# Kernel tuning notes

Measured on AMD Instinct MI355X. Metric: run time of the kernel, lower is better.

## Reference

```python
import jax, jax.numpy as jnp
import numpy as np

D_MODEL = 1024
N_HEADS = 16
D_K = D_MODEL // N_HEADS
LN_EPS = 1e-5


def setup_inputs() -> dict:
    key = jax.random.key(0)
    ks = jax.random.split(key, 11)
    s = 1.0 / np.sqrt(D_MODEL)
    x = jax.random.normal(ks[0], (4, 2048, D_MODEL), dtype=jnp.float32)
    W_q = jax.random.uniform(ks[1], (D_MODEL, D_MODEL), jnp.float32, -s, s)
    b_q = jax.random.uniform(ks[2], (D_MODEL,), jnp.float32, -s, s)
    W_k = jax.random.uniform(ks[3], (D_MODEL, D_MODEL), jnp.float32, -s, s)
    b_k = jax.random.uniform(ks[4], (D_MODEL,), jnp.float32, -s, s)
    W_v = jax.random.uniform(ks[5], (D_MODEL, D_MODEL), jnp.float32, -s, s)
    b_v = jax.random.uniform(ks[6], (D_MODEL,), jnp.float32, -s, s)
    W_o = jax.random.uniform(ks[7], (D_MODEL, D_MODEL), jnp.float32, -s, s)
    b_o = jax.random.uniform(ks[8], (D_MODEL,), jnp.float32, -s, s)
    ln_gamma = jnp.ones((D_MODEL,), jnp.float32)
    ln_beta = jnp.zeros((D_MODEL,), jnp.float32)
    return {"x": x, "W_q": W_q, "b_q": b_q, "W_k": W_k, "b_k": b_k,
            "W_v": W_v, "b_v": b_v, "W_o": W_o, "b_o": b_o,
            "ln_gamma": ln_gamma, "ln_beta": ln_beta}


def reference(x, W_q, b_q, W_k, b_k, W_v, b_v, W_o, b_o, ln_gamma, ln_beta):
    B, S, D = x.shape
    # Linear projections (torch Linear: x @ W.T + b); split into heads.
    def proj(W, b):
        y = jnp.einsum('bsd,ed->bse', x, W) + b
        return y.reshape(B, S, N_HEADS, D_K).transpose(0, 2, 1, 3)  # [B,H,S,dk]
    Q = proj(W_q, b_q)
    K = proj(W_k, b_k)
    V = proj(W_v, b_v)
    scores = jnp.einsum('bhqd,bhkd->bhqk', Q, K) / np.sqrt(D_K)
    attn = jax.nn.softmax(scores, axis=-1)  # dropout is identity in eval
    context = jnp.einsum('bhqk,bhkd->bhqd', attn, V)
    context = context.transpose(0, 2, 1, 3).reshape(B, S, D)
    out = jnp.einsum('bsd,ed->bse', context, W_o) + b_o
    h = x + out  # residual
    mu = jnp.mean(h, axis=-1, keepdims=True)
    var = jnp.mean(jnp.square(h - mu), axis=-1, keepdims=True)
    return (h - mu) / jnp.sqrt(var + LN_EPS) * ln_gamma + ln_beta
```

## Files before the change

### kernel.cpp

```cpp
#include <hip/hip_runtime.h>
#include <hip/hip_bf16.h>
#include <stdint.h>

typedef __attribute__((ext_vector_type(4))) float f32x4;
typedef __attribute__((ext_vector_type(8))) short bf16x8;
typedef __attribute__((ext_vector_type(4))) short bf16x4;
typedef __attribute__((ext_vector_type(4))) short s16x4;

__device__ __forceinline__ float b2f(short s) {
    union { uint32_t u; float f; } v; v.u = ((uint32_t)(uint16_t)s) << 16; return v.f;
}
__device__ __forceinline__ short f2b(float f) {
    union { float f; uint32_t u; } v; v.f = f;
    uint32_t r = v.u + 0x7FFF + ((v.u >> 16) & 1);
    return (short)(r >> 16);
}
__device__ __forceinline__ f32x4 zero4() { f32x4 z = {0.f, 0.f, 0.f, 0.f}; return z; }

__device__ __forceinline__ void async16(const void* g, void* l) {
    __builtin_amdgcn_global_load_lds(
        (const __attribute__((address_space(1))) void*)g,
        (__attribute__((address_space(3))) void*)l, 16, 0, 0);
}
__device__ __forceinline__ uint32_t lds_addr(const void* p) {
    return (uint32_t)(uintptr_t)(const __attribute__((address_space(3))) void*)p;
}
__device__ __forceinline__ float exp2fast(float x) {
    float r; asm("v_exp_f32 %0, %1" : "=v"(r) : "v"(x)); return r;
}
__device__ __forceinline__ uint32_t cvtpk(float lo, float hi) {
    uint32_t r; asm("v_cvt_pk_bf16_f32 %0, %1, %2" : "=v"(r) : "v"(lo), "v"(hi)); return r;
}

__global__ __launch_bounds__(256)
void cvt5(const float* __restrict__ x,
          const float* __restrict__ wq, const float* __restrict__ wk,
          const float* __restrict__ wv, const float* __restrict__ wo,
          short* __restrict__ xb, short* __restrict__ wqb, short* __restrict__ wkb,
          short* __restrict__ wvb, short* __restrict__ wob)
{
    const int b = blockIdx.x;
    const float* src; short* dst; size_t off;
    if (b < 8192) { src = x; dst = xb; off = (size_t)b * 1024; }
    else {
        const int wsel = (b - 8192) >> 10;
        off = (size_t)((b - 8192) & 1023) * 1024;
        switch (wsel) {
            case 0: src = wq; dst = wqb; break;
            case 1: src = wk; dst = wkb; break;
            case 2: src = wv; dst = wvb; break;
            default: src = wo; dst = wob; break;
        }
    }
    const int t = threadIdx.x;
    const float4 v = *(const float4*)(src + off + t * 4);
    s16x4 o;
    o[0] = f2b(v.x); o[1] = f2b(v.y); o[2] = f2b(v.z); o[3] = f2b(v.w);
    *(s16x4*)(dst + off + t * 4) = o;
}

template <bool OUTF32, bool RESID>
__device__ __forceinline__
void gemm_core(const short* __restrict__ Ab, const short* __restrict__ Bb,
               const float* __restrict__ bias, const float* __restrict__ resid,
               void* __restrict__ Cv, int m0, int n0col, int K, int N,
               short* lsA, short* lsB)
{
    const int t = threadIdx.x;
    const int wave = t >> 6, lane = t & 63;
    const int wr = wave >> 1, wc = wave & 1;
    const int lr = lane & 15, kg = lane >> 4;

    f32x4 acc[4][4];
#pragma unroll
    for (int m = 0; m < 4; ++m)
#pragma unroll
        for (int n = 0; n < 4; ++n) acc[m][n] = zero4();

    const int rG = t >> 3;
    const int cG = (((t & 7) ^ (rG & 7))) * 8;

    for (int k0 = 0; k0 < K; k0 += 64) {
        __syncthreads();
#pragma unroll
        for (int i = 0; i < 4; ++i) {
            async16(Ab + (size_t)(rG + 32 * i) * K + k0 + cG, &lsA[t * 8 + 2048 * i]);
            async16(Bb + (size_t)(rG + 32 * i) * K + k0 + cG, &lsB[t * 8 + 2048 * i]);
        }
        __syncthreads();

#pragma unroll
        for (int ks = 0; ks < 2; ++ks) {
            const int xc = ((ks * 4 + kg) ^ (lr & 7)) * 8;
            bf16x8 aF[4], bF[4];
#pragma unroll
            for (int m = 0; m < 4; ++m)
                aF[m] = *(const bf16x8*)&lsA[(wr * 64 + m * 16 + lr) * 64 + xc];
#pragma unroll
            for (int n = 0; n < 4; ++n)
                bF[n] = *(const bf16x8*)&lsB[(wc * 64 + n * 16 + lr) * 64 + xc];
#pragma unroll
            for (int m = 0; m < 4; ++m)
#pragma unroll
                for (int n = 0; n < 4; ++n)
                    acc[m][n] = __builtin_amdgcn_mfma_f32_16x16x32_bf16(aF[m], bF[n], acc[m][n], 0, 0, 0);
        }
    }

#pragma unroll
    for (int n = 0; n < 4; ++n) {
        const int col = n0col + wc * 64 + n * 16 + lr;
        const float bvv = bias[col];
#pragma unroll
        for (int m = 0; m < 4; ++m) {
            const int rowb = m0 + wr * 64 + m * 16 + kg * 4;
#pragma unroll
            for (int r = 0; r < 4; ++r) {
                const size_t idx = (size_t)(rowb + r) * N + col;
                float v = acc[m][n][r] + bvv;
                if (RESID) v += resid[idx];
                if (OUTF32) ((float*)Cv)[idx] = v;
                else        ((short*)Cv)[idx] = f2b(v);
            }
        }
    }
}

__global__ __launch_bounds__(256)
void gemm_qkv(const short* __restrict__ A, const short* __restrict__ Wcat,
              const float* __restrict__ bq, const float* __restrict__ bk,
              const float* __restrict__ bv,
              short* __restrict__ Qw, short* __restrict__ Kw, short* __restrict__ Vw)
{
    __shared__ short lsA[128 * 64];
    __shared__ short lsB[128 * 64];
    const int nb = blockIdx.x;
    const int tb = nb >> 3;
    const float* bias = (tb == 0) ? bq : (tb == 1) ? bk : bv;
    short* dst = (tb == 0) ? Qw : (tb == 1) ? Kw : Vw;
    gemm_core<false, false>(A + (size_t)blockIdx.y * 128 * 1024,
                            Wcat + (size_t)nb * 128 * 1024,
                            bias - (nb & 7) * 128,
                            nullptr, dst, blockIdx.y * 128, (nb & 7) * 128, 1024, 1024,
                            lsA, lsB);
}

__global__ __launch_bounds__(256)
void gemm_out(const short* __restrict__ A, const short* __restrict__ Bw,
              const float* __restrict__ bias, const float* __restrict__ resid,
              float* __restrict__ C)
{
    __shared__ short lsA[128 * 64];
    __shared__ short lsB[128 * 64];
    gemm_core<true, true>(A + (size_t)blockIdx.y * 128 * 1024,
                          Bw + (size_t)blockIdx.x * 128 * 1024,
                          bias, resid, C, blockIdx.y * 128, blockIdx.x * 128, 1024, 1024,
                          lsA, lsB);
}

__global__ __launch_bounds__(512)
void attn_fwd(const short* __restrict__ Q, const short* __restrict__ K,
              const short* __restrict__ V, short* __restrict__ ctx)
{
    __shared__ short lsK[2][64 * 64];
    __shared__ short lsV[2][64 * 64];
    __shared__ short lsP[8][16 * 64];

    const float C1 = 0.18033688011112042f;

    const int t = threadIdx.x, w = t >> 6, lane = t & 63;
    const int lr = lane & 15, kg = lane >> 4;
    const int bh = blockIdx.x;
    const size_t base = (size_t)(bh >> 4) * 2048 * 1024 + (size_t)(bh & 15) * 64;
    const short* Qg = Q + base;
    short* Og = ctx + base;
    const int q0 = blockIdx.y * 256 + w * 32;

    bf16x8 qB[2][2];
#pragma unroll
    for (int m = 0; m < 2; ++m)
#pragma unroll
        for (int ks = 0; ks < 2; ++ks)
            qB[m][ks] = *(const bf16x8*)(Qg + (size_t)(q0 + m * 16 + lr) * 1024 + ks * 32 + kg * 8);

    const int rK  = t >> 3;
    const int cK  = (((t & 7) ^ (rK & 7))) * 8;
    const int kvV = (t & 127) >> 1;
    const int dV  = ((t >> 7) << 4) + (t & 1) * 8;
    const short* pK = K + base + (size_t)rK * 1024 + cK;
    const short* pV = V + base + (size_t)kvV * 1024 + dV;

    f32x4 o[2][4];
#pragma unroll
    for (int m = 0; m < 2; ++m)
#pragma unroll
        for (int n = 0; n < 4; ++n) o[m][n] = zero4();
    float mx[2] = {-1e30f, -1e30f};
    float lsum[2] = {0.f, 0.f};

    const int pmask = (lr & 7) << 3;
    short* lsPw = lsP[w];

    async16(pK, &lsK[0][t * 8]);
    async16(pV, &lsV[0][t * 8]);

    int buf = 0;
    for (int it = 0; it < 32; ++it) {
        __syncthreads();
        if (it + 1 < 32) {
            pK += 65536; pV += 65536;
            async16(pK, &lsK[buf ^ 1][t * 8]);
            async16(pV, &lsV[buf ^ 1][t * 8]);
        }
        const short* cbK = lsK[buf];
        const short* cbV = lsV[buf];

        f32x4 s[2][4];
        const int x0 = ((kg)     ^ (lr & 7)) * 8;
        const int x1 = ((4 + kg) ^ (lr & 7)) * 8;
        __builtin_amdgcn_s_setprio(1);
#pragma unroll
        for (int cb = 0; cb < 4; ++cb) {
            const bf16x8 kA0 = *(const bf16x8*)&cbK[(cb * 16 + lr) * 64 + x0];
            const bf16x8 kA1 = *(const bf16x8*)&cbK[(cb * 16 + lr) * 64 + x1];
#pragma unroll
            for (int m = 0; m < 2; ++m) {
                f32x4 a = __builtin_amdgcn_mfma_f32_16x16x32_bf16(kA0, qB[m][0], zero4(), 0, 0, 0);
                s[m][cb] = __builtin_amdgcn_mfma_f32_16x16x32_bf16(kA1, qB[m][1], a, 0, 0, 0);
            }
        }
        __builtin_amdgcn_s_setprio(0);

        float smax[2];
#pragma unroll
        for (int m = 0; m < 2; ++m) {
            float a = fmaxf(fmaxf(s[m][0][0], s[m][0][1]), fmaxf(s[m][0][2], s[m][0][3]));
            float b = fmaxf(fmaxf(s[m][1][0], s[m][1][1]), fmaxf(s[m][1][2], s[m][1][3]));
            float c = fmaxf(fmaxf(s[m][2][0], s[m][2][1]), fmaxf(s[m][2][2], s[m][2][3]));
            float d = fmaxf(fmaxf(s[m][3][0], s[m][3][1]), fmaxf(s[m][3][2], s[m][3][3]));
            float e = fmaxf(fmaxf(a, b), fmaxf(c, d));
            e = fmaxf(e, __shfl_xor(e, 16));
            e = fmaxf(e, __shfl_xor(e, 32));
            smax[m] = e;
        }

        if (!__all((smax[0] <= mx[0] + 64.f) && (smax[1] <= mx[1] + 64.f))) {
            float corrS[2];
#pragma unroll
            for (int m = 0; m < 2; ++m) {
                const float mnew = fmaxf(mx[m], smax[m]);
                corrS[m] = exp2fast((mx[m] - mnew) * C1);
                mx[m] = mnew;
                lsum[m] *= corrS[m];
            }
#pragma unroll
            for (int m = 0; m < 2; ++m) {
                f32x4 c;
#pragma unroll
                for (int r = 0; r < 4; ++r) c[r] = __shfl(corrS[m], kg * 4 + r);
#pragma unroll
                for (int n = 0; n < 4; ++n) {
                    o[m][n][0] *= c[0]; o[m][n][1] *= c[1];
                    o[m][n][2] *= c[2]; o[m][n][3] *= c[3];
                }
            }
        }

        bf16x4 tv[4][4];
#pragma unroll
        for (int n = 0; n < 4; ++n) {
            const uint32_t a = lds_addr(&cbV[n * 1024 + kg * 128 + lr]);
            asm volatile(
                "ds_read_b64_tr_b16 %0, %4\n\t"
                "ds_read_b64_tr_b16 %1, %4 offset:128\n\t"
                "ds_read_b64_tr_b16 %2, %4 offset:1024\n\t"
                "ds_read_b64_tr_b16 %3, %4 offset:1152"
                : "=&v"(tv[n][0]), "=&v"(tv[n][1]), "=&v"(tv[n][2]), "=&v"(tv[n][3])
                : "v"(a));
        }
        asm volatile("s_waitcnt lgkmcnt(0)" ::: "memory");
        __builtin_amdgcn_sched_barrier(0);

#pragma unroll
        for (int m = 0; m < 2; ++m) {
            const float nm2 = mx[m] * C1;
            float tsum = 0.f;
#pragma unroll
            for (int cb = 0; cb < 4; ++cb) {
                const float p0 = exp2fast(fmaf(s[m][cb][0], C1, -nm2));
                const float p1 = exp2fast(fmaf(s[m][cb][1], C1, -nm2));
                const float p2 = exp2fast(fmaf(s[m][cb][2], C1, -nm2));
                const float p3 = exp2fast(fmaf(s[m][cb][3], C1, -nm2));
                tsum += (p0 + p1) + (p2 + p3);
                const int c0i = (cb * 16 + kg * 4) ^ pmask;
                *(uint32_t*)&lsPw[lr * 64 + c0i]     = cvtpk(p0, p1);
                *(uint32_t*)&lsPw[lr * 64 + c0i + 2] = cvtpk(p2, p3);
            }
            lsum[m] += tsum;

            bf16x8 pA[2];
#pragma unroll
            for (int kh = 0; kh < 2; ++kh)
                pA[kh] = *(const bf16x8*)&lsPw[lr * 64 + ((kh * 32 + kg * 8) ^ pmask)];

            __builtin_amdgcn_s_setprio(1);
#pragma unroll
            for (int n = 0; n < 4; ++n) {
#pragma unroll
                for (int kh = 0; kh < 2; ++kh) {
                    const bf16x8 vB = __builtin_shufflevector(tv[n][kh * 2], tv[n][kh * 2 + 1],
                                                              0, 1, 2, 3, 4, 5, 6, 7);
                    o[m][n] = __builtin_amdgcn_mfma_f32_16x16x32_bf16(pA[kh], vB, o[m][n], 0, 0, 0);
                }
            }
            __builtin_amdgcn_s_setprio(0);
        }
        buf ^= 1;
    }

#pragma unroll
    for (int m = 0; m < 2; ++m) {
        float lp = lsum[m];
        lp += __shfl_xor(lp, 16);
        lp += __shfl_xor(lp, 32);
        f32x4 inv;
#pragma unroll
        for (int r = 0; r < 4; ++r) inv[r] = 1.0f / __shfl(lp, kg * 4 + r);
#pragma unroll
        for (int n = 0; n < 4; ++n)
#pragma unroll
            for (int r = 0; r < 4; ++r) {
                const int row = q0 + m * 16 + kg * 4 + r;
                Og[(size_t)row * 1024 + n * 16 + lr] = f2b(o[m][n][r] * inv[r]);
            }
    }
}

__global__ __launch_bounds__(256)
void ln_inplace(float* __restrict__ io, const float* __restrict__ gamma,
                const float* __restrict__ beta)
{
    __shared__ float redS[4];
    __shared__ float redQ[4];
    const int t = threadIdx.x, wave = t >> 6, lane = t & 63;
    const size_t rb = (size_t)blockIdx.x * 1024;

    float4 v4 = *(const float4*)&io[rb + t * 4];
    float v[4] = {v4.x, v4.y, v4.z, v4.w};

    float s = 0.f, sq = 0.f;
#pragma unroll
    for (int j = 0; j < 4; ++j) { s += v[j]; sq += v[j] * v[j]; }
#pragma unroll
    for (int off = 32; off; off >>= 1) {
        s  += __shfl_xor(s, off);
        sq += __shfl_xor(sq, off);
    }
    if (lane == 0) { redS[wave] = s; redQ[wave] = sq; }
    __syncthreads();
    const float mean = (redS[0] + redS[1] + redS[2] + redS[3]) * (1.0f / 1024.0f);
    const float ex2  = (redQ[0] + redQ[1] + redQ[2] + redQ[3]) * (1.0f / 1024.0f);
    const float var  = fmaxf(ex2 - mean * mean, 0.f);
    const float inv  = rsqrtf(var + 1e-5f);

    float4 o4;
    o4.x = (v[0] - mean) * inv * gamma[t * 4 + 0] + beta[t * 4 + 0];
    o4.y = (v[1] - mean) * inv * gamma[t * 4 + 1] + beta[t * 4 + 1];
    o4.z = (v[2] - mean) * inv * gamma[t * 4 + 2] + beta[t * 4 + 2];
    o4.w = (v[3] - mean) * inv * gamma[t * 4 + 3] + beta[t * 4 + 3];
    *(float4*)&io[rb + t * 4] = o4;
}

extern "C" void kernel_launch(void* const* d_in, const int* in_sizes, int n_in,
                              void* d_out, int out_size, void* d_ws, size_t ws_size,
                              hipStream_t stream)
{
    const float* x  = (const float*)d_in[0];
    const float* Wq = (const float*)d_in[1];
    const float* bq = (const float*)d_in[2];
    const float* Wk = (const float*)d_in[3];
    const float* bk = (const float*)d_in[4];
    const float* Wv = (const float*)d_in[5];
    const float* bv = (const float*)d_in[6];
    const float* Wo = (const float*)d_in[7];
    const float* bo = (const float*)d_in[8];
    const float* gamma = (const float*)d_in[9];
    const float* beta  = (const float*)d_in[10];

    const size_t NX = (size_t)8192 * 1024;
    const size_t NW = (size_t)1024 * 1024;

    short* xb  = (short*)d_ws;
    short* Wqb = xb + NX;
    short* Wkb = Wqb + NW;
    short* Wvb = Wkb + NW;
    short* Wob = Wvb + NW;
    short* Qw  = Wob + NW;
    short* Kw  = Qw + NX;
    short* Vw  = Kw + NX;
    short* Cw  = Vw + NX;
    float* out = (float*)d_out;

    cvt5<<<dim3(12288), dim3(256), 0, stream>>>(x, Wq, Wk, Wv, Wo, xb, Wqb, Wkb, Wvb, Wob);
    gemm_qkv<<<dim3(24, 64), dim3(256), 0, stream>>>(xb, Wqb, bq, bk, bv, Qw, Kw, Vw);
    attn_fwd<<<dim3(64, 8), dim3(512), 0, stream>>>(Qw, Kw, Vw, Cw);
    gemm_out<<<dim3(8, 64), dim3(256), 0, stream>>>(Cw, Wob, bo, x, out);
    ln_inplace<<<dim3(8192), dim3(256), 0, stream>>>(out, gamma, beta);
}
```

Measured before the change: 243.5 us.

## Remap GEMM workgroups per XCD and compute softmax row sums via MFMA

Both GEMM kernels now launch a 1D grid and remap each block index so that consecutive tiles go to the same XCD (blocks are assigned round-robin over 8 XCDs). The aim is better L2 reuse of the A and B tiles. The attention kernel drops the scalar row-sum accumulation and its cross-lane shuffles. It instead multiplies the bf16 P tile by a ones vector with two extra MFMAs per row block, which moves the reduction onto the matrix units. The row sums now come from bf16-rounded probabilities, so they match what multiplies V, at the cost of extra MFMA work.

```diff
diff --git a/kernel.cpp b/kernel.cpp
--- a/kernel.cpp
+++ b/kernel.cpp
@@ -134,14 +134,17 @@
 {
     __shared__ short lsA[128 * 64];
     __shared__ short lsB[128 * 64];
-    const int nb = blockIdx.x;
+    const int L = blockIdx.x;
+    const int wgid = (L & 7) * 192 + (L >> 3);
+    const int nb = wgid % 24;
+    const int my = wgid / 24;
     const int tb = nb >> 3;
     const float* bias = (tb == 0) ? bq : (tb == 1) ? bk : bv;
     short* dst = (tb == 0) ? Qw : (tb == 1) ? Kw : Vw;
-    gemm_core<false, false>(A + (size_t)blockIdx.y * 128 * 1024,
+    gemm_core<false, false>(A + (size_t)my * 128 * 1024,
                             Wcat + (size_t)nb * 128 * 1024,
                             bias - (nb & 7) * 128,
-                            nullptr, dst, blockIdx.y * 128, (nb & 7) * 128, 1024, 1024,
+                            nullptr, dst, my * 128, (nb & 7) * 128, 1024, 1024,
                             lsA, lsB);
 }
 
@@ -152,9 +155,12 @@
 {
     __shared__ short lsA[128 * 64];
     __shared__ short lsB[128 * 64];
-    gemm_core<true, true>(A + (size_t)blockIdx.y * 128 * 1024,
-                          Bw + (size_t)blockIdx.x * 128 * 1024,
-                          bias, resid, C, blockIdx.y * 128, blockIdx.x * 128, 1024, 1024,
+    const int L = blockIdx.x;
+    const int wgid = (L & 7) * 64 + (L >> 3);
+    const int nb = wgid & 7, my = wgid >> 3;
+    gemm_core<true, true>(A + (size_t)my * 128 * 1024,
+                          Bw + (size_t)nb * 128 * 1024,
+                          bias, resid, C, my * 128, nb * 128, 1024, 1024,
                           lsA, lsB);
 }
 
@@ -183,6 +189,10 @@
         for (int ks = 0; ks < 2; ++ks)
             qB[m][ks] = *(const bf16x8*)(Qg + (size_t)(q0 + m * 16 + lr) * 1024 + ks * 32 + kg * 8);
 
+    bf16x8 onesB;
+#pragma unroll
+    for (int j = 0; j < 8; ++j) onesB[j] = (short)0x3F80;
+
     const int rK  = t >> 3;
     const int cK  = (((t & 7) ^ (rK & 7))) * 8;
     const int kvV = (t & 127) >> 1;
@@ -191,12 +201,14 @@
     const short* pV = V + base + (size_t)kvV * 1024 + dV;
 
     f32x4 o[2][4];
-#pragma unroll
-    for (int m = 0; m < 2; ++m)
+    f32x4 osum[2];
+#pragma unroll
+    for (int m = 0; m < 2; ++m) {
 #pragma unroll
         for (int n = 0; n < 4; ++n) o[m][n] = zero4();
+        osum[m] = zero4();
+    }
     float mx[2] = {-1e30f, -1e30f};
-    float lsum[2] = {0.f, 0.f};
 
     const int pmask = (lr & 7) << 3;
     short* lsPw = lsP[w];
@@ -251,7 +263,6 @@
                 const float mnew = fmaxf(mx[m], smax[m]);
                 corrS[m] = exp2fast((mx[m] - mnew) * C1);
                 mx[m] = mnew;
-                lsum[m] *= corrS[m];
             }
 #pragma unroll
             for (int m = 0; m < 2; ++m) {
@@ -263,6 +274,8 @@
                     o[m][n][0] *= c[0]; o[m][n][1] *= c[1];
                     o[m][n][2] *= c[2]; o[m][n][3] *= c[3];
                 }
+                osum[m][0] *= c[0]; osum[m][1] *= c[1];
+                osum[m][2] *= c[2]; osum[m][3] *= c[3];
             }
         }
 
@@ -284,19 +297,16 @@
 #pragma unroll
         for (int m = 0; m < 2; ++m) {
             const float nm2 = mx[m] * C1;
-            float tsum = 0.f;
 #pragma unroll
             for (int cb = 0; cb < 4; ++cb) {
                 const float p0 = exp2fast(fmaf(s[m][cb][0], C1, -nm2));
                 const float p1 = exp2fast(fmaf(s[m][cb][1], C1, -nm2));
                 const float p2 = exp2fast(fmaf(s[m][cb][2], C1, -nm2));
                 const float p3 = exp2fast(fmaf(s[m][cb][3], C1, -nm2));
-                tsum += (p0 + p1) + (p2 + p3);
                 const int c0i = (cb * 16 + kg * 4) ^ pmask;
                 *(uint32_t*)&lsPw[lr * 64 + c0i]     = cvtpk(p0, p1);
                 *(uint32_t*)&lsPw[lr * 64 + c0i + 2] = cvtpk(p2, p3);
             }
-            lsum[m] += tsum;
 
             bf16x8 pA[2];
 #pragma unroll
@@ -313,6 +323,8 @@
                     o[m][n] = __builtin_amdgcn_mfma_f32_16x16x32_bf16(pA[kh], vB, o[m][n], 0, 0, 0);
                 }
             }
+            osum[m] = __builtin_amdgcn_mfma_f32_16x16x32_bf16(pA[0], onesB, osum[m], 0, 0, 0);
+            osum[m] = __builtin_amdgcn_mfma_f32_16x16x32_bf16(pA[1], onesB, osum[m], 0, 0, 0);
             __builtin_amdgcn_s_setprio(0);
         }
         buf ^= 1;
@@ -320,12 +332,9 @@
 
 #pragma unroll
     for (int m = 0; m < 2; ++m) {
-        float lp = lsum[m];
-        lp += __shfl_xor(lp, 16);
-        lp += __shfl_xor(lp, 32);
         f32x4 inv;
 #pragma unroll
-        for (int r = 0; r < 4; ++r) inv[r] = 1.0f / __shfl(lp, kg * 4 + r);
+        for (int r = 0; r < 4; ++r) inv[r] = 1.0f / osum[m][r];
 #pragma unroll
         for (int n = 0; n < 4; ++n)
 #pragma unroll
@@ -402,8 +411,8 @@
     float* out = (float*)d_out;
 
     cvt5<<<dim3(12288), dim3(256), 0, stream>>>(x, Wq, Wk, Wv, Wo, xb, Wqb, Wkb, Wvb, Wob);
-    gemm_qkv<<<dim3(24, 64), dim3(256), 0, stream>>>(xb, Wqb, bq, bk, bv, Qw, Kw, Vw);
+    gemm_qkv<<<dim3(1536), dim3(256), 0, stream>>>(xb, Wqb, bq, bk, bv, Qw, Kw, Vw);
     attn_fwd<<<dim3(64, 8), dim3(512), 0, stream>>>(Qw, Kw, Vw, Cw);
-    gemm_out<<<dim3(8, 64), dim3(256), 0, stream>>>(Cw, Wob, bo, x, out);
+    gemm_out<<<dim3(512), dim3(256), 0, stream>>>(Cw, Wob, bo, x, out);
     ln_inplace<<<dim3(8192), dim3(256), 0, stream>>>(out, gamma, beta);
 }
```

Result: no change. 239.4 us (-1.7%).
